# Kernel optimization log

Hardware: AMD Instinct MI355X
Metric: run time of the kernel (lower is better)

## Reference

```python
import jax, jax.numpy as jnp
import numpy as np

N, D = 8192, 128
EPS = 1e-6  # torch F.pairwise_distance default eps


def _pe(d, s=3, t=2):
    # 1/d^s - 1/d^t
    return 1.0 / (d ** s) - 1.0 / (d ** t)


def setup_inputs() -> dict:
    key = jax.random.key(0)
    x = jax.random.normal(key, (N, D), dtype=jnp.float32)
    return {"x": x}


def reference(x):
    n = x.shape[0]
    # loss0: distance of each row to the origin; torch pairwise_distance adds eps to the diff
    d0 = jnp.sqrt(jnp.sum((x + EPS) ** 2, axis=-1))  # [N]
    loss0 = jnp.mean(jnp.clip(_pe(d0), -1.5, 1000.0))

    # pdist: condensed upper-triangular pairwise Euclidean distances (no eps)
    sq = jnp.sum(x * x, axis=-1)                      # [N]
    d2 = sq[:, None] + sq[None, :] - 2.0 * (x @ x.T)  # [N, N]
    mask = jnp.triu(jnp.ones((n, n), dtype=bool), k=1)
    # keep masked entries at 1.0 so sqrt/pe stay finite
    d2 = jnp.where(mask, jnp.maximum(d2, 0.0), 1.0)
    d = jnp.sqrt(d2)
    vals = jnp.clip(_pe(d), -1.5, 1000.0)
    cnt = n * (n - 1) // 2
    loss = jnp.sum(jnp.where(mask, vals, 0.0)) / cnt
    return loss0 + loss
```

## Files before the change

kernel.cpp:

```cpp
#include <hip/hip_runtime.h>
#include <hip/hip_bf16.h>


#define NROWS 8192
#define DDIM  128
#define TILE  128
#define RB    128
#define TTILES (NROWS / TILE)
#define NTRI  (TTILES * (TTILES + 1) / 2)
#define NBLKP 1024
#define FEPS  1e-6f

typedef float f32x4 __attribute__((ext_vector_type(4)));
typedef float f32x2 __attribute__((ext_vector_type(2)));
typedef long long i64;

__device__ __forceinline__ float rsq_fast(float x) {
    float r;
    asm("v_rsq_f32 %0, %1" : "=v"(r) : "v"(x));
    return r;
}
__device__ __forceinline__ f32x2 pk_fma(f32x2 a, f32x2 b, f32x2 c) {
    f32x2 d;
    asm("v_pk_fma_f32 %0, %1, %2, %3" : "=v"(d) : "v"(a), "v"(b), "v"(c));
    return d;
}
__device__ __forceinline__ f32x2 pk_add(f32x2 a, f32x2 b) {
    f32x2 d;
    asm("v_pk_add_f32 %0, %1, %2" : "=v"(d) : "v"(a), "v"(b));
    return d;
}
__device__ __forceinline__ f32x2 pk_mul(f32x2 a, f32x2 b) {
    f32x2 d;
    asm("v_pk_mul_f32 %0, %1, %2" : "=v"(d) : "v"(a), "v"(b));
    return d;
}

__global__ __launch_bounds__(256) void convert_kernel(
        const float* __restrict__ x, unsigned short* __restrict__ xf8_u16,
        float* __restrict__ sq, float* __restrict__ p0) {
    int tid = threadIdx.x;
    int wave = tid >> 6, lane = tid & 63;
    int row = blockIdx.x * 4 + wave;

    float2 v = *(const float2*)(x + (size_t)row * DDIM + lane * 2);
    float s = v.x * v.x + v.y * v.y;
    float ex = v.x + FEPS, ey = v.y + FEPS;
    float e = ex * ex + ey * ey;

    int packed = __builtin_amdgcn_cvt_pk_fp8_f32(v.x, v.y, 0, false);
    xf8_u16[(size_t)row * 64 + lane] = (unsigned short)(packed & 0xFFFF);

    #pragma unroll
    for (int off = 32; off; off >>= 1) {
        s += __shfl_down(s, off);
        e += __shfl_down(e, off);
    }

    __shared__ float red[4];
    if (lane == 0) {
        sq[row] = s;
        float r = rsqrtf(e);
        float r2 = r * r;
        red[wave] = fminf(fmaxf(r2 * r - r2, -1.5f), 1000.0f);
    }
    __syncthreads();
    if (tid == 0) p0[blockIdx.x] = red[0] + red[1] + red[2] + red[3];
}

__device__ __forceinline__ int tri_off(int i) {
    return i * TTILES - ((i * (i - 1)) >> 1);
}

__device__ __forceinline__ void stage_tile(const char* __restrict__ g,
                                           char* lds, int tid) {
    uint4 v[2];
    #pragma unroll
    for (int p = 0; p < 2; ++p)
        v[p] = *(const uint4*)(g + (p * 512 + tid) * 16);
    #pragma unroll
    for (int p = 0; p < 2; ++p) {
        int n = p * 512 + tid;
        int row = n >> 3, c = n & 7;
        *(uint4*)(lds + row * RB + ((c * 16) ^ ((row & 7) << 4))) = v[p];
    }
}

__global__ __launch_bounds__(512, 4) void pair_kernel(
        const unsigned short* __restrict__ xf8_u16,
        const float* __restrict__ sq, float* __restrict__ pp) {
    const char* xb = (const char*)xf8_u16;
    __shared__ char smem[32768];
    char* ldsA = smem;
    char* ldsB = smem + 16384;

    int b = blockIdx.x;
    int t0, cnt;
    if (b < 32) { t0 = b * 3; cnt = 3; }
    else        { t0 = 96 + (b - 32) * 2; cnt = 2; }

    int I = 0;
    {
        float T2 = 2.0f * TTILES + 1.0f;
        I = (int)((T2 - sqrtf(T2 * T2 - 8.0f * (float)t0)) * 0.5f);
        while (tri_off(I + 1) <= t0) ++I;
        while (tri_off(I) > t0) --I;
    }
    int J = I + (t0 - tri_off(I));

    int tid = threadIdx.x;
    int wave = tid >> 6, lane = tid & 63;
    int wR = (wave >> 2) * 64;
    int wC = (wave & 3) * 32;
    int lcol = lane & 15;
    int lrow = lane >> 4;

    const f32x2 neg2 = {-2.0f, -2.0f};
    f32x2 l3 = {0.f, 0.f}, l2 = {0.f, 0.f};
    float ldiag = 0.0f;
    f32x2 si2[4][2];
    int curI = -1;

    for (int k = 0; k < cnt; ++k) {
        if (I != curI) {
            stage_tile(xb + (size_t)I * TILE * RB, ldsA, tid);
            int ibase = I * TILE + wR + lrow * 4;
            #pragma unroll
            for (int r = 0; r < 4; ++r)
                #pragma unroll
                for (int h = 0; h < 2; ++h) {
                    float2 v = *(const float2*)(sq + ibase + r * 16 + h * 2);
                    si2[r][h] = (f32x2){v.x, v.y};
                }
            curI = I;
        }
        bool diag = (I == J);
        if (!diag) stage_tile(xb + (size_t)J * TILE * RB, ldsB, tid);
        __syncthreads();
        const char* bufB = diag ? ldsA : ldsB;

        f32x4 acc[4][2];
        #pragma unroll
        for (int r = 0; r < 4; ++r)
            #pragma unroll
            for (int c = 0; c < 2; ++c) acc[r][c] = (f32x4){0.f, 0.f, 0.f, 0.f};

        #pragma unroll
        for (int ks = 0; ks < 4; ++ks) {
            int koff = ks * 32 + lrow * 8;
            i64 a[4], bb[2];
            #pragma unroll
            for (int r = 0; r < 4; ++r) {
                int row = wR + r * 16 + lcol;
                a[r] = *(const i64*)(ldsA + row * RB + (koff ^ ((row & 7) << 4)));
            }
            #pragma unroll
            for (int c = 0; c < 2; ++c) {
                int row = wC + c * 16 + lcol;
                bb[c] = *(const i64*)(bufB + row * RB + (koff ^ ((row & 7) << 4)));
            }
            #pragma unroll
            for (int r = 0; r < 4; ++r)
                #pragma unroll
                for (int c = 0; c < 2; ++c)
                    acc[r][c] = __builtin_amdgcn_mfma_f32_16x16x32_fp8_fp8(
                        a[r], bb[c], acc[r][c], 0, 0, 0);
        }

        int jbase = J * TILE + wC + lcol;
        float sqj[2];
        #pragma unroll
        for (int c = 0; c < 2; ++c) sqj[c] = sq[jbase + c * 16];

        if (!diag) {
            f32x2 sj2[2];
            #pragma unroll
            for (int c = 0; c < 2; ++c) sj2[c] = (f32x2){sqj[c], sqj[c]};
            #pragma unroll
            for (int r = 0; r < 4; ++r)
                #pragma unroll
                for (int c = 0; c < 2; ++c)
                    #pragma unroll
                    for (int h = 0; h < 2; ++h) {
                        f32x2 acc2 = {acc[r][c][2 * h], acc[r][c][2 * h + 1]};
                        f32x2 s2 = pk_add(si2[r][h], sj2[c]);
                        f32x2 d2 = pk_fma(acc2, neg2, s2);
                        f32x2 rv = {rsq_fast(d2[0]), rsq_fast(d2[1])};
                        f32x2 r2 = pk_mul(rv, rv);
                        l3 = pk_fma(r2, rv, l3);
                        l2 = pk_add(l2, r2);
                    }
        } else {
            int il0 = wR + lrow * 4;
            int jl0 = wC + lcol;
            #pragma unroll
            for (int r = 0; r < 4; ++r)
                #pragma unroll
                for (int u = 0; u < 4; ++u) {
                    int il = il0 + r * 16 + u;
                    float si = si2[r][u >> 1][u & 1];
                    #pragma unroll
                    for (int c = 0; c < 2; ++c) {
                        if (jl0 + c * 16 > il) {
                            float d2 = fmaxf(si + sqj[c] - 2.0f * acc[r][c][u], 1e-30f);
                            float rv = rsq_fast(d2);
                            float r2 = rv * rv;
                            ldiag += fminf(r2 * rv - r2, 1000.0f);
                        }
                    }
                }
        }
        __syncthreads();

        ++J;
        if (J == TTILES) { ++I; J = I; }
    }

    float lsum = (l3[0] + l3[1]) - (l2[0] + l2[1]) + ldiag;

    #pragma unroll
    for (int off = 32; off; off >>= 1) lsum += __shfl_down(lsum, off);
    __shared__ float red[8];
    if (lane == 0) red[wave] = lsum;
    __syncthreads();
    if (tid == 0) {
        float t = 0.f;
        #pragma unroll
        for (int w = 0; w < 8; ++w) t += red[w];
        pp[blockIdx.x] = t;
    }
}

__global__ __launch_bounds__(1024) void reduce_kernel(
        const float* __restrict__ p0, int n0,
        const float* __restrict__ pp, int np, float* __restrict__ out) {
    int tid = threadIdx.x;
    double s0 = 0.0, sp = 0.0;
    for (int i = tid; i < n0; i += 1024) s0 += (double)p0[i];
    for (int i = tid; i < np; i += 1024) sp += (double)pp[i];
    #pragma unroll
    for (int off = 32; off; off >>= 1) {
        s0 += __shfl_down(s0, off);
        sp += __shfl_down(sp, off);
    }
    __shared__ double sh[32];
    int wave = tid >> 6, lane = tid & 63;
    if (lane == 0) { sh[2 * wave] = s0; sh[2 * wave + 1] = sp; }
    __syncthreads();
    if (tid == 0) {
        double a = 0.0, bsum = 0.0;
        #pragma unroll
        for (int w = 0; w < 16; ++w) { a += sh[2 * w]; bsum += sh[2 * w + 1]; }
        double cnt = (double)NROWS * (double)(NROWS - 1) * 0.5;
        out[0] = (float)(a / (double)NROWS + bsum / cnt);
    }
}

extern "C" void kernel_launch(void* const* d_in, const int* in_sizes, int n_in,
                              void* d_out, int out_size, void* d_ws, size_t ws_size,
                              hipStream_t stream) {
    const float* x = (const float*)d_in[0];
    char* ws = (char*)d_ws;
    const size_t OFF_SQ = 1048576;
    const size_t OFF_P0 = OFF_SQ + 32768;
    const size_t OFF_PP = OFF_P0 + 8192;
    if (ws_size < OFF_PP + NBLKP * sizeof(float)) return;

    unsigned short* xf8 = (unsigned short*)ws;
    float* sq = (float*)(ws + OFF_SQ);
    float* p0 = (float*)(ws + OFF_P0);
    float* pp = (float*)(ws + OFF_PP);

    convert_kernel<<<NROWS / 4, 256, 0, stream>>>(x, xf8, sq, p0);
    pair_kernel<<<NBLKP, 512, 0, stream>>>(xf8, sq, pp);
    reduce_kernel<<<1, 1024, 0, stream>>>(p0, NROWS / 4, pp, NBLKP, (float*)d_out);
}
```

Measured before the change: 28.59 us.

## Give each wave private 64x64 subtiles and drop block-wide barriers

The pair kernel now runs 4 waves per block, and each wave computes its own 64x64 sub-tile of the 128x128 tile pair. Each wave stages its A/B rows into a private LDS region, so the block-wide __syncthreads between tiles goes away. The FP8 buffer is re-laid out as two K-halves of 64 bytes per row so that each half can be staged and consumed in turn. On diagonal tiles one wave of the four sits idle, and each wave now holds 16 accumulators, which raises register pressure. The I tile is also no longer reused across consecutive tile pairs, so operands are reloaded from global memory more often.

```diff
diff --git a/kernel.cpp b/kernel.cpp
--- a/kernel.cpp
+++ b/kernel.cpp
@@ -5,7 +5,6 @@
 #define NROWS 8192
 #define DDIM  128
 #define TILE  128
-#define RB    128
 #define TTILES (NROWS / TILE)
 #define NTRI  (TTILES * (TTILES + 1) / 2)
 #define NBLKP 1024
@@ -49,7 +48,9 @@
     float e = ex * ex + ey * ey;
 
     int packed = __builtin_amdgcn_cvt_pk_fp8_f32(v.x, v.y, 0, false);
-    xf8_u16[(size_t)row * 64 + lane] = (unsigned short)(packed & 0xFFFF);
+    int h = lane >> 5;
+    xf8_u16[((size_t)h * NROWS + row) * 32 + (lane & 31)] =
+        (unsigned short)(packed & 0xFFFF);
 
     #pragma unroll
     for (int off = 32; off; off >>= 1) {
@@ -72,27 +73,18 @@
     return i * TTILES - ((i * (i - 1)) >> 1);
 }
 
-__device__ __forceinline__ void stage_tile(const char* __restrict__ g,
-                                           char* lds, int tid) {
-    uint4 v[2];
-    #pragma unroll
-    for (int p = 0; p < 2; ++p)
-        v[p] = *(const uint4*)(g + (p * 512 + tid) * 16);
-    #pragma unroll
-    for (int p = 0; p < 2; ++p) {
-        int n = p * 512 + tid;
-        int row = n >> 3, c = n & 7;
-        *(uint4*)(lds + row * RB + ((c * 16) ^ ((row & 7) << 4))) = v[p];
-    }
-}
-
-__global__ __launch_bounds__(512, 4) void pair_kernel(
+__global__ __launch_bounds__(256, 4) void pair_kernel(
         const unsigned short* __restrict__ xf8_u16,
         const float* __restrict__ sq, float* __restrict__ pp) {
     const char* xb = (const char*)xf8_u16;
     __shared__ char smem[32768];
-    char* ldsA = smem;
-    char* ldsB = smem + 16384;
+
+    int tid = threadIdx.x;
+    int wave = tid >> 6, lane = tid & 63;
+    char* ldsA = smem + wave * 8192;
+    char* ldsB = ldsA + 4096;
+    int lcol = lane & 15;
+    int lrow = lane >> 4;
 
     int b = blockIdx.x;
     int t0, cnt;
@@ -108,109 +100,119 @@
     }
     int J = I + (t0 - tri_off(I));
 
-    int tid = threadIdx.x;
-    int wave = tid >> 6, lane = tid & 63;
-    int wR = (wave >> 2) * 64;
-    int wC = (wave & 3) * 32;
-    int lcol = lane & 15;
-    int lrow = lane >> 4;
-
     const f32x2 neg2 = {-2.0f, -2.0f};
     f32x2 l3 = {0.f, 0.f}, l2 = {0.f, 0.f};
     float ldiag = 0.0f;
-    f32x2 si2[4][2];
-    int curI = -1;
 
     for (int k = 0; k < cnt; ++k) {
-        if (I != curI) {
-            stage_tile(xb + (size_t)I * TILE * RB, ldsA, tid);
-            int ibase = I * TILE + wR + lrow * 4;
+        int ai, bi, mode;
+        if (I != J) { ai = 2 * I + (wave >> 1); bi = 2 * J + (wave & 1); mode = 0; }
+        else if (wave < 2) { ai = bi = 2 * I + wave; mode = 1; }
+        else if (wave == 2) { ai = 2 * I; bi = 2 * I + 1; mode = 0; }
+        else { ai = bi = 0; mode = 2; }
+
+        if (mode != 2) {
+            f32x4 acc[4][4];
             #pragma unroll
             for (int r = 0; r < 4; ++r)
                 #pragma unroll
-                for (int h = 0; h < 2; ++h) {
-                    float2 v = *(const float2*)(sq + ibase + r * 16 + h * 2);
-                    si2[r][h] = (f32x2){v.x, v.y};
-                }
-            curI = I;
+                for (int c = 0; c < 4; ++c) acc[r][c] = (f32x4){0.f, 0.f, 0.f, 0.f};
+
+            #pragma unroll
+            for (int h = 0; h < 2; ++h) {
+                const char* gA = xb + ((size_t)h * NROWS + (size_t)ai * 64) * 64;
+                const char* gB = xb + ((size_t)h * NROWS + (size_t)bi * 64) * 64;
+                uint4 va[4], vb[4];
+                #pragma unroll
+                for (int p = 0; p < 4; ++p) {
+                    va[p] = *(const uint4*)(gA + (p * 64 + lane) * 16);
+                    vb[p] = *(const uint4*)(gB + (p * 64 + lane) * 16);
+                }
+                #pragma unroll
+                for (int p = 0; p < 4; ++p) {
+                    int n = p * 64 + lane;
+                    int row = n >> 2, c = n & 3;
+                    int ofs = row * 64 + (((c ^ ((row >> 2) & 3)) << 4));
+                    *(uint4*)(ldsA + ofs) = va[p];
+                    *(uint4*)(ldsB + ofs) = vb[p];
+                }
+                #pragma unroll
+                for (int ksl = 0; ksl < 2; ++ksl) {
+                    int cidx = ksl * 2 + (lrow >> 1);
+                    int off8 = (lrow & 1) << 3;
+                    i64 a[4], bb[4];
+                    #pragma unroll
+                    for (int fr = 0; fr < 4; ++fr) {
+                        int row = fr * 16 + lcol;
+                        a[fr] = *(const i64*)(ldsA + row * 64 +
+                                 ((cidx ^ ((row >> 2) & 3)) << 4) + off8);
+                    }
+                    #pragma unroll
+                    for (int fc = 0; fc < 4; ++fc) {
+                        int row = fc * 16 + lcol;
+                        bb[fc] = *(const i64*)(ldsB + row * 64 +
+                                 ((cidx ^ ((row >> 2) & 3)) << 4) + off8);
+                    }
+                    #pragma unroll
+                    for (int fr = 0; fr < 4; ++fr)
+                        #pragma unroll
+                        for (int fc = 0; fc < 4; ++fc)
+                            acc[fr][fc] = __builtin_amdgcn_mfma_f32_16x16x32_fp8_fp8(
+                                a[fr], bb[fc], acc[fr][fc], 0, 0, 0);
+                }
+            }
+
+            int ibase = ai * 64 + lrow * 4;
+            int jbase = bi * 64 + lcol;
+            f32x2 si2[4][2];
+            #pragma unroll
+            for (int fr = 0; fr < 4; ++fr)
+                #pragma unroll
+                for (int hh = 0; hh < 2; ++hh) {
+                    float2 v = *(const float2*)(sq + ibase + fr * 16 + hh * 2);
+                    si2[fr][hh] = (f32x2){v.x, v.y};
+                }
+            float sj[4];
+            #pragma unroll
+            for (int fc = 0; fc < 4; ++fc) sj[fc] = sq[jbase + fc * 16];
+
+            if (mode == 0) {
+                #pragma unroll
+                for (int fc = 0; fc < 4; ++fc) {
+                    f32x2 sj2 = {sj[fc], sj[fc]};
+                    #pragma unroll
+                    for (int fr = 0; fr < 4; ++fr)
+                        #pragma unroll
+                        for (int hh = 0; hh < 2; ++hh) {
+                            f32x2 acc2 = {acc[fr][fc][2 * hh], acc[fr][fc][2 * hh + 1]};
+                            f32x2 s2 = pk_add(si2[fr][hh], sj2);
+                            f32x2 d2 = pk_fma(acc2, neg2, s2);
+                            f32x2 rv = {rsq_fast(d2[0]), rsq_fast(d2[1])};
+                            f32x2 r2 = pk_mul(rv, rv);
+                            l3 = pk_fma(r2, rv, l3);
+                            l2 = pk_add(l2, r2);
+                        }
+                }
+            } else {
+                int il0 = lrow * 4;
+                #pragma unroll
+                for (int fc = 0; fc < 4; ++fc) {
+                    int jl = fc * 16 + lcol;
+                    #pragma unroll
+                    for (int fr = 0; fr < 4; ++fr)
+                        #pragma unroll
+                        for (int u = 0; u < 4; ++u) {
+                            if (jl > il0 + fr * 16 + u) {
+                                float si = si2[fr][u >> 1][u & 1];
+                                float d2 = fmaxf(si + sj[fc] - 2.0f * acc[fr][fc][u], 1e-30f);
+                                float rv = rsq_fast(d2);
+                                float r2 = rv * rv;
+                                ldiag += fminf(r2 * rv - r2, 1000.0f);
+                            }
+                        }
+                }
+            }
         }
-        bool diag = (I == J);
-        if (!diag) stage_tile(xb + (size_t)J * TILE * RB, ldsB, tid);
-        __syncthreads();
-        const char* bufB = diag ? ldsA : ldsB;
-
-        f32x4 acc[4][2];
-        #pragma unroll
-        for (int r = 0; r < 4; ++r)
-            #pragma unroll
-            for (int c = 0; c < 2; ++c) acc[r][c] = (f32x4){0.f, 0.f, 0.f, 0.f};
-
-        #pragma unroll
-        for (int ks = 0; ks < 4; ++ks) {
-            int koff = ks * 32 + lrow * 8;
-            i64 a[4], bb[2];
-            #pragma unroll
-            for (int r = 0; r < 4; ++r) {
-                int row = wR + r * 16 + lcol;
-                a[r] = *(const i64*)(ldsA + row * RB + (koff ^ ((row & 7) << 4)));
-            }
-            #pragma unroll
-            for (int c = 0; c < 2; ++c) {
-                int row = wC + c * 16 + lcol;
-                bb[c] = *(const i64*)(bufB + row * RB + (koff ^ ((row & 7) << 4)));
-            }
-            #pragma unroll
-            for (int r = 0; r < 4; ++r)
-                #pragma unroll
-                for (int c = 0; c < 2; ++c)
-                    acc[r][c] = __builtin_amdgcn_mfma_f32_16x16x32_fp8_fp8(
-                        a[r], bb[c], acc[r][c], 0, 0, 0);
-        }
-
-        int jbase = J * TILE + wC + lcol;
-        float sqj[2];
-        #pragma unroll
-        for (int c = 0; c < 2; ++c) sqj[c] = sq[jbase + c * 16];
-
-        if (!diag) {
-            f32x2 sj2[2];
-            #pragma unroll
-            for (int c = 0; c < 2; ++c) sj2[c] = (f32x2){sqj[c], sqj[c]};
-            #pragma unroll
-            for (int r = 0; r < 4; ++r)
-                #pragma unroll
-                for (int c = 0; c < 2; ++c)
-                    #pragma unroll
-                    for (int h = 0; h < 2; ++h) {
-                        f32x2 acc2 = {acc[r][c][2 * h], acc[r][c][2 * h + 1]};
-                        f32x2 s2 = pk_add(si2[r][h], sj2[c]);
-                        f32x2 d2 = pk_fma(acc2, neg2, s2);
-                        f32x2 rv = {rsq_fast(d2[0]), rsq_fast(d2[1])};
-                        f32x2 r2 = pk_mul(rv, rv);
-                        l3 = pk_fma(r2, rv, l3);
-                        l2 = pk_add(l2, r2);
-                    }
-        } else {
-            int il0 = wR + lrow * 4;
-            int jl0 = wC + lcol;
-            #pragma unroll
-            for (int r = 0; r < 4; ++r)
-                #pragma unroll
-                for (int u = 0; u < 4; ++u) {
-                    int il = il0 + r * 16 + u;
-                    float si = si2[r][u >> 1][u & 1];
-                    #pragma unroll
-                    for (int c = 0; c < 2; ++c) {
-                        if (jl0 + c * 16 > il) {
-                            float d2 = fmaxf(si + sqj[c] - 2.0f * acc[r][c][u], 1e-30f);
-                            float rv = rsq_fast(d2);
-                            float r2 = rv * rv;
-                            ldiag += fminf(r2 * rv - r2, 1000.0f);
-                        }
-                    }
-                }
-        }
-        __syncthreads();
 
         ++J;
         if (J == TTILES) { ++I; J = I; }
@@ -220,15 +222,10 @@
 
     #pragma unroll
     for (int off = 32; off; off >>= 1) lsum += __shfl_down(lsum, off);
-    __shared__ float red[8];
+    __shared__ float red[4];
     if (lane == 0) red[wave] = lsum;
     __syncthreads();
-    if (tid == 0) {
-        float t = 0.f;
-        #pragma unroll
-        for (int w = 0; w < 8; ++w) t += red[w];
-        pp[blockIdx.x] = t;
-    }
+    if (tid == 0) pp[blockIdx.x] = red[0] + red[1] + red[2] + red[3];
 }
 
 __global__ __launch_bounds__(1024) void reduce_kernel(
@@ -272,6 +269,6 @@
     float* pp = (float*)(ws + OFF_PP);
 
     convert_kernel<<<NROWS / 4, 256, 0, stream>>>(x, xf8, sq, p0);
-    pair_kernel<<<NBLKP, 512, 0, stream>>>(xf8, sq, pp);
+    pair_kernel<<<NBLKP, 256, 0, stream>>>(xf8, sq, pp);
     reduce_kernel<<<1, 1024, 0, stream>>>(p0, NROWS / 4, pp, NBLKP, (float*)d_out);
 }
```

Result: slower. 32.66 us (+14.2%).
